# Optimization experiments

Hardware: AMD Instinct MI355X
Metric: run time of the kernel (lower is better)

## Reference

```python
import jax, jax.numpy as jnp
import numpy as np

EMBED_DIM = 768
NUM_HEADS = 12
MAX_LEN = 512
BATCH = 8
SEQ = 512
HEAD_DIM = EMBED_DIM // NUM_HEADS


def setup_inputs() -> dict:
    key = jax.random.key(0)
    ks = jax.random.split(key, 7)
    x = jax.random.normal(ks[0], (BATCH, SEQ, EMBED_DIM), dtype=jnp.float32)
    mask = jnp.ones((BATCH, SEQ), dtype=jnp.int32)
    Wq = jax.random.normal(ks[1], (EMBED_DIM, EMBED_DIM), dtype=jnp.float32) * (1.0 / np.sqrt(EMBED_DIM))
    Wk = jax.random.normal(ks[2], (EMBED_DIM, EMBED_DIM), dtype=jnp.float32) * (1.0 / np.sqrt(EMBED_DIM))
    Wv = jax.random.normal(ks[3], (EMBED_DIM, EMBED_DIM), dtype=jnp.float32) * (1.0 / np.sqrt(EMBED_DIM))
    rel_pos = jax.random.normal(ks[4], (2 * MAX_LEN - 1, NUM_HEADS), dtype=jnp.float32)
    Wo = jax.random.normal(ks[5], (EMBED_DIM, EMBED_DIM), dtype=jnp.float32) * (1.0 / np.sqrt(EMBED_DIM))
    bo = jax.random.normal(ks[6], (EMBED_DIM,), dtype=jnp.float32) * 0.02
    return {"x": x, "mask": mask, "Wq": Wq, "Wk": Wk, "Wv": Wv,
            "rel_pos": rel_pos, "Wo": Wo, "bo": bo}


def reference(x, mask, Wq, Wk, Wv, rel_pos, Wo, bo):
    B, S, E = x.shape
    H, D = NUM_HEADS, HEAD_DIM
    Q = (x @ Wq).reshape(B, S, H, D)
    K = (x @ Wk).reshape(B, S, H, D)
    V = (x @ Wv).reshape(B, S, H, D)
    # scores: [B, H, S, S]
    scores = jnp.einsum('bqhd,bkhd->bhqk', Q, K) / np.sqrt(D).astype(np.float32)
    # relative position bias: idx[q,k] = k - q + max_len - 1, clamped
    pos = jnp.arange(S)
    idx = jnp.clip(pos[None, :] - pos[:, None] + MAX_LEN - 1, 0, 2 * MAX_LEN - 2)
    bias = rel_pos[idx]                       # [S, S, H]
    scores = scores + jnp.transpose(bias, (2, 0, 1))[None]  # [1,H,S,S]
    # mask: b i * b j -> [B,1,S,S]
    m2 = (mask[:, None, :, None] * mask[:, None, None, :]) != 0
    mask_value = -jnp.finfo(scores.dtype).max
    scores = jnp.where(m2, scores, mask_value)
    attn = jax.nn.softmax(scores, axis=-1)
    out = jnp.einsum('bhqk,bkhd->bqhd', attn, V).reshape(B, S, E)
    out = out @ Wo + bo  # dropout is identity in eval mode
    return out
```

## Files before the change

kernel.cpp:

```cpp
#include <hip/hip_runtime.h>
#include <hip/hip_bf16.h>
#include <cfloat>
#include <cstdint>
#include <cmath>

#define EMBED 768
#define NHEAD 12
#define SEQB  8
#define SEQ   512
#define HDIM  64
#define WMAT  589824

typedef __attribute__((ext_vector_type(8))) short short8;
typedef __attribute__((ext_vector_type(4))) short short4v;
typedef __attribute__((ext_vector_type(4))) float f32x4;

__device__ __forceinline__ short f2bf(float f) {
  uint32_t u = __float_as_uint(f);
  u += 0x7FFF + ((u >> 16) & 1u);
  return (short)(u >> 16);
}

__device__ __forceinline__ short f2bf1(float f) {
  int r;
  asm("v_cvt_pk_bf16_f32 %0, %1, %2" : "=v"(r) : "v"(f), "v"(f));
  return (short)r;
}

__device__ __forceinline__ void gload_lds16(const void* g, void* l) {
  __builtin_amdgcn_global_load_lds((const __attribute__((address_space(1))) void*)g,
                                   (__attribute__((address_space(3))) void*)l, 16, 0, 0);
}

__global__ void k_cast_x(const float* __restrict__ x, short* __restrict__ xb) {
  int i = blockIdx.x * blockDim.x + threadIdx.x;
  const int n4 = SEQB * SEQ * EMBED / 4;
  if (i < n4) {
    float4 v = ((const float4*)x)[i];
    short4v o;
    o.x = f2bf(v.x); o.y = f2bf(v.y); o.z = f2bf(v.z); o.w = f2bf(v.w);
    ((short4v*)xb)[i] = o;
  }
}

__global__ void k_cast_wt(const float* __restrict__ Wq, const float* __restrict__ Wk,
                          const float* __restrict__ Wv, const float* __restrict__ Wo,
                          short* __restrict__ Wt) {
  __shared__ float tile[32][33];
  const int mat = blockIdx.z;
  const float* src = (mat == 0) ? Wq : (mat == 1) ? Wk : (mat == 2) ? Wv : Wo;
  const int n0 = blockIdx.x * 32, k0 = blockIdx.y * 32;
  const int tx = threadIdx.x & 31, ty = threadIdx.x >> 5;
  #pragma unroll
  for (int rr = 0; rr < 4; rr++)
    tile[ty + rr * 8][tx] = src[(size_t)(k0 + ty + rr * 8) * EMBED + n0 + tx];
  __syncthreads();
  short* dst = Wt + (size_t)mat * WMAT;
  #pragma unroll
  for (int rr = 0; rr < 4; rr++)
    dst[(size_t)(n0 + ty + rr * 8) * EMBED + k0 + tx] = f2bf(tile[tx][ty + rr * 8]);
}

template <int MODE>
__launch_bounds__(256)
__global__ void k_gemm(const short* __restrict__ A, const short* __restrict__ B,
                       short* __restrict__ O0, short* __restrict__ O1,
                       short* __restrict__ O2,
                       float* __restrict__ OF, const float* __restrict__ bias) {
  __shared__ __attribute__((aligned(16))) short As[128 * 32];
  __shared__ __attribute__((aligned(16))) short Bs[128 * 32];
  const int tid = threadIdx.x;
  const int lane = tid & 63, w = tid >> 6;
  const int g = lane >> 4, c = lane & 15;
  const int wi = (w >> 1) * 64, wj = (w & 1) * 64;
  const int i0 = blockIdx.y * 128, j0 = blockIdx.x * 128;

  f32x4 acc[4][4];
  #pragma unroll
  for (int a = 0; a < 4; a++)
    #pragma unroll
    for (int b2 = 0; b2 < 4; b2++) acc[a][b2] = (f32x4){0.f, 0.f, 0.f, 0.f};

  for (int k0 = 0; k0 < EMBED; k0 += 32) {
    if (k0) __syncthreads();
    #pragma unroll
    for (int it = 0; it < 2; it++) {
      int gi = tid + it * 256;
      int row = gi >> 2, q = gi & 3;
      gload_lds16(A + (size_t)(i0 + row) * EMBED + k0 + q * 8, As + gi * 8);
      gload_lds16(B + (size_t)(j0 + row) * EMBED + k0 + q * 8, Bs + gi * 8);
    }
    __syncthreads();
    short8 aF[4], bF[4];
    #pragma unroll
    for (int mi = 0; mi < 4; mi++) aF[mi] = *(const short8*)&As[(wi + mi * 16 + c) * 32 + g * 8];
    #pragma unroll
    for (int nj = 0; nj < 4; nj++) bF[nj] = *(const short8*)&Bs[(wj + nj * 16 + c) * 32 + g * 8];
    #pragma unroll
    for (int mi = 0; mi < 4; mi++)
      #pragma unroll
      for (int nj = 0; nj < 4; nj++)
        acc[mi][nj] = __builtin_amdgcn_mfma_f32_16x16x32_bf16(aF[mi], bF[nj], acc[mi][nj], 0, 0, 0);
  }

  #pragma unroll
  for (int mi = 0; mi < 4; mi++) {
    int i = i0 + wi + mi * 16 + 4 * g;
    #pragma unroll
    for (int nj = 0; nj < 4; nj++) {
      int j = j0 + wj + nj * 16 + c;
      f32x4 v = acc[mi][nj];
      if (MODE == 0) {
        int n = i, m = j;
        int b = m >> 9, s = m & 511;
        if (n < 1536) {
          short* dst = O0; int nn = n;
          if (n >= 768) { dst = O1; nn -= 768; }
          int h = nn >> 6, d = nn & 63;
          short4v o; o.x = f2bf(v.x); o.y = f2bf(v.y); o.z = f2bf(v.z); o.w = f2bf(v.w);
          *(short4v*)&dst[(size_t)(((b * 12 + h) * 512 + s) * 64 + d)] = o;
        } else {
          int nn = n - 1536;
          int h = nn >> 6, d = nn & 63;
          size_t base = ((size_t)(b * 12 + h) * 64 + d) * 512 + s;
          O2[base] = f2bf(v.x); O2[base + 512] = f2bf(v.y);
          O2[base + 1024] = f2bf(v.z); O2[base + 1536] = f2bf(v.w);
        }
      } else {
        int n = i, m = j;
        float4 bb = *(const float4*)&bias[n];
        float4 o; o.x = v.x + bb.x; o.y = v.y + bb.y; o.z = v.z + bb.z; o.w = v.w + bb.w;
        *(float4*)&OF[(size_t)m * EMBED + n] = o;
      }
    }
  }
}

__launch_bounds__(256)
__global__ void k_attn(const short* __restrict__ Q, const short* __restrict__ K,
                       const short* __restrict__ Vt, const int* __restrict__ mask,
                       const float* __restrict__ rel_pos, short* __restrict__ attO) {
  __shared__ float bias_lds[1024];
  __shared__ int mask_lds[512];
  __shared__ __attribute__((aligned(16))) short Plds[4][16 * 32];
  __shared__ __attribute__((aligned(16))) short Kbuf[2][32 * 64];
  __shared__ __attribute__((aligned(16))) short Vbuf[2][64 * 32];
  const int tid = threadIdx.x;
  const int lane = tid & 63, w = tid >> 6;
  const int g = lane >> 4, c = lane & 15;
  const int bid = blockIdx.x;
  const int q0 = (bid / 96) * 64;
  const int bh = bid % 96;
  const int b = bh / 12, h = bh % 12;
  const short* Qb = Q + (size_t)bh * (512 * 64);
  const short* Kb = K + (size_t)bh * (512 * 64);
  const short* Vb = Vt + (size_t)bh * (64 * 512);

  const float LOG2E = 1.44269504089f;
  for (int i = tid; i < 1023; i += 256) bias_lds[i] = (rel_pos[i * 12 + h] - 16.0f) * LOG2E;
  for (int i = tid; i < 512; i += 256) mask_lds[i] = mask[b * 512 + i];

  const int krow_s = tid >> 3, kc_s = tid & 7;
  const int vrow_s = tid >> 2, vc_s = tid & 3;
  #define STAGEKV(T, BUF)                                                             \
    {                                                                                 \
      gload_lds16(Kb + ((T) * 32 + krow_s) * 64 + (kc_s ^ (krow_s & 7)) * 8,          \
                  &Kbuf[BUF][tid * 8]);                                               \
      gload_lds16(Vb + (size_t)vrow_s * 512 + (T) * 32 + (vc_s ^ ((vrow_s >> 1) & 3)) * 8, \
                  &Vbuf[BUF][tid * 8]);                                               \
    }

  STAGEKV(0, 0)

  short8 qf[2];
  #pragma unroll
  for (int dc = 0; dc < 2; dc++)
    qf[dc] = *(const short8*)&Qb[(q0 + w * 16 + c) * 64 + dc * 32 + g * 8];

  __syncthreads();

  int qrow[4], mq[4], bbase[4];
  #pragma unroll
  for (int r = 0; r < 4; r++) {
    qrow[r] = q0 + w * 16 + 4 * g + r;
    mq[r] = mask_lds[qrow[r]];
    bbase[r] = 511 - qrow[r];
  }

  float l_part[4];
  f32x4 accO[4];
  #pragma unroll
  for (int r = 0; r < 4; r++) l_part[r] = 0.f;
  #pragma unroll
  for (int dt = 0; dt < 4; dt++) accO[dt] = (f32x4){0.f, 0.f, 0.f, 0.f};

  const float SC = 0.125f * 1.44269504089f;
  short* Pw = &Plds[w][0];
  const int rdoff = c * 32 + g * 8;
  const int kswz = c & 7;
  const int vswz = (c >> 1) & 3;

  int bufsel = 0;
  for (int t = 0; t < 16; ++t) {
    if (t < 15) STAGEKV(t + 1, bufsel ^ 1)
    const short* Kt = &Kbuf[bufsel][0];
    const short* Vs = &Vbuf[bufsel][0];

    short8 kf[4], vf[4];
    #pragma unroll
    for (int ct = 0; ct < 2; ct++)
      #pragma unroll
      for (int dc = 0; dc < 2; dc++)
        kf[ct * 2 + dc] = *(const short8*)&Kt[(ct * 16 + c) * 64 + ((dc * 4 + g) ^ kswz) * 8];
    #pragma unroll
    for (int dt = 0; dt < 4; dt++)
      vf[dt] = *(const short8*)&Vs[(dt * 16 + c) * 32 + ((g ^ vswz)) * 8];

    f32x4 s0 = (f32x4){0.f, 0.f, 0.f, 0.f}, s1 = s0;
    s0 = __builtin_amdgcn_mfma_f32_16x16x32_bf16(qf[0], kf[0], s0, 0, 0, 0);
    s0 = __builtin_amdgcn_mfma_f32_16x16x32_bf16(qf[1], kf[1], s0, 0, 0, 0);
    s1 = __builtin_amdgcn_mfma_f32_16x16x32_bf16(qf[0], kf[2], s1, 0, 0, 0);
    s1 = __builtin_amdgcn_mfma_f32_16x16x32_bf16(qf[1], kf[3], s1, 0, 0, 0);

    float p_[2][4];
    {
      const int krow = t * 32 + c;
      const int mk0 = mask_lds[krow], mk1 = mask_lds[krow + 16];
      #pragma unroll
      for (int r = 0; r < 4; r++) {
        float a0 = fmaf(s0[r], SC, bias_lds[krow + bbase[r]]);
        float a1 = fmaf(s1[r], SC, bias_lds[krow + 16 + bbase[r]]);
        float p0 = exp2f(a0), p1 = exp2f(a1);
        if ((mq[r] & mk0) == 0) p0 = 0.f;
        if ((mq[r] & mk1) == 0) p1 = 0.f;
        p_[0][r] = p0; p_[1][r] = p1;
        l_part[r] += p0 + p1;
      }
    }
    #pragma unroll
    for (int ct = 0; ct < 2; ct++)
      #pragma unroll
      for (int r = 0; r < 4; r++)
        Pw[(4 * g + r) * 32 + ct * 16 + c] = f2bf1(p_[ct][r]);
    short8 pa = *(const short8*)&Pw[rdoff];
    #pragma unroll
    for (int dt = 0; dt < 4; dt++)
      accO[dt] = __builtin_amdgcn_mfma_f32_16x16x32_bf16(pa, vf[dt], accO[dt], 0, 0, 0);

    __syncthreads();
    bufsel ^= 1;
  }

  float inv[4];
  #pragma unroll
  for (int r = 0; r < 4; r++) {
    float lr = l_part[r];
    #pragma unroll
    for (int off = 1; off < 16; off <<= 1) lr += __shfl_xor(lr, off);
    inv[r] = 1.0f / lr;
  }
  #pragma unroll
  for (int dt = 0; dt < 4; dt++)
    #pragma unroll
    for (int r = 0; r < 4; r++)
      attO[(size_t)(b * 512 + qrow[r]) * EMBED + h * 64 + dt * 16 + c] =
          f2bf(accO[dt][r] * inv[r]);
}

extern "C" void kernel_launch(void* const* d_in, const int* in_sizes, int n_in,
                              void* d_out, int out_size, void* d_ws, size_t ws_size,
                              hipStream_t stream) {
  const float* x = (const float*)d_in[0];
  const int* mask = (const int*)d_in[1];
  const float* Wq = (const float*)d_in[2];
  const float* Wk = (const float*)d_in[3];
  const float* Wv = (const float*)d_in[4];
  const float* rel_pos = (const float*)d_in[5];
  const float* Wo = (const float*)d_in[6];
  const float* bo = (const float*)d_in[7];
  float* out = (float*)d_out;

  char* ws = (char*)d_ws;
  short* xb = (short*)ws;
  short* Wt = (short*)(ws + 6291456);
  short* Qg = (short*)(ws + 6291456 + 4718592);
  short* Kg = Qg + 3145728;
  short* Vt = Kg + 3145728;
  short* attO = xb;

  k_cast_x<<<3072, 256, 0, stream>>>(x, xb);
  k_cast_wt<<<dim3(24, 24, 4), 256, 0, stream>>>(Wq, Wk, Wv, Wo, Wt);
  k_gemm<0><<<dim3(32, 18), 256, 0, stream>>>(Wt, xb, Qg, Kg, Vt, nullptr, nullptr);
  k_attn<<<768, 256, 0, stream>>>(Qg, Kg, Vt, mask, rel_pos, attO);
  k_gemm<2><<<dim3(32, 6), 256, 0, stream>>>(Wt + 3 * WMAT, attO, nullptr, nullptr, nullptr, out, bo);
}
```

Before: 153.8 us.

## Double-buffer GEMM LDS tiles and use partial vmcnt waits in attention

The projection GEMM now stages its A/B tiles into two LDS buffers, prefetching the next K-step while computing the current one. It uses s_waitcnt vmcnt(N) with raw s_barrier instead of full __syncthreads. The attention kernel's K/V double-buffering likewise switches to partial vmcnt waits, so the prefetch for tile t+1 can stay in flight while tile t is consumed. This targets exposed global-load latency, at the cost of doubled GEMM LDS use and correctness that depends on hand-counted outstanding-load numbers.

```diff
diff --git a/kernel.cpp b/kernel.cpp
--- a/kernel.cpp
+++ b/kernel.cpp
@@ -67,13 +67,14 @@
                        short* __restrict__ O0, short* __restrict__ O1,
                        short* __restrict__ O2,
                        float* __restrict__ OF, const float* __restrict__ bias) {
-  __shared__ __attribute__((aligned(16))) short As[128 * 32];
-  __shared__ __attribute__((aligned(16))) short Bs[128 * 32];
+  __shared__ __attribute__((aligned(16))) short As[2][128 * 32];
+  __shared__ __attribute__((aligned(16))) short Bs[2][128 * 32];
   const int tid = threadIdx.x;
   const int lane = tid & 63, w = tid >> 6;
   const int g = lane >> 4, c = lane & 15;
   const int wi = (w >> 1) * 64, wj = (w & 1) * 64;
   const int i0 = blockIdx.y * 128, j0 = blockIdx.x * 128;
+  const int NSTEP = EMBED / 32;
 
   f32x4 acc[4][4];
   #pragma unroll
@@ -81,26 +82,45 @@
     #pragma unroll
     for (int b2 = 0; b2 < 4; b2++) acc[a][b2] = (f32x4){0.f, 0.f, 0.f, 0.f};
 
-  for (int k0 = 0; k0 < EMBED; k0 += 32) {
-    if (k0) __syncthreads();
-    #pragma unroll
-    for (int it = 0; it < 2; it++) {
-      int gi = tid + it * 256;
-      int row = gi >> 2, q = gi & 3;
-      gload_lds16(A + (size_t)(i0 + row) * EMBED + k0 + q * 8, As + gi * 8);
-      gload_lds16(B + (size_t)(j0 + row) * EMBED + k0 + q * 8, Bs + gi * 8);
-    }
-    __syncthreads();
+  #define GSTAGE(S, BUF)                                                            \
+    { _Pragma("unroll")                                                             \
+      for (int it = 0; it < 2; it++) {                                              \
+        int gi = tid + it * 256;                                                    \
+        int row = gi >> 2, qq = gi & 3;                                             \
+        gload_lds16(A + (size_t)(i0 + row) * EMBED + (S) * 32 + qq * 8,             \
+                    &As[BUF][gi * 8]);                                              \
+        gload_lds16(B + (size_t)(j0 + row) * EMBED + (S) * 32 + qq * 8,             \
+                    &Bs[BUF][gi * 8]);                                              \
+      } }
+
+  GSTAGE(0, 0)
+  __syncthreads();
+
+  for (int s = 0; s < NSTEP; ++s) {
+    const int cur = s & 1;
+    if (s < NSTEP - 1) {
+      GSTAGE(s + 1, cur ^ 1)
+      asm volatile("s_waitcnt vmcnt(4)" ::: "memory");
+    } else {
+      asm volatile("s_waitcnt vmcnt(0)" ::: "memory");
+    }
+    __builtin_amdgcn_sched_barrier(0);
+    __builtin_amdgcn_s_barrier();
+    __builtin_amdgcn_sched_barrier(0);
+
     short8 aF[4], bF[4];
     #pragma unroll
-    for (int mi = 0; mi < 4; mi++) aF[mi] = *(const short8*)&As[(wi + mi * 16 + c) * 32 + g * 8];
-    #pragma unroll
-    for (int nj = 0; nj < 4; nj++) bF[nj] = *(const short8*)&Bs[(wj + nj * 16 + c) * 32 + g * 8];
+    for (int mi = 0; mi < 4; mi++) aF[mi] = *(const short8*)&As[cur][(wi + mi * 16 + c) * 32 + g * 8];
+    #pragma unroll
+    for (int nj = 0; nj < 4; nj++) bF[nj] = *(const short8*)&Bs[cur][(wj + nj * 16 + c) * 32 + g * 8];
     #pragma unroll
     for (int mi = 0; mi < 4; mi++)
       #pragma unroll
       for (int nj = 0; nj < 4; nj++)
         acc[mi][nj] = __builtin_amdgcn_mfma_f32_16x16x32_bf16(aF[mi], bF[nj], acc[mi][nj], 0, 0, 0);
+
+    __builtin_amdgcn_s_barrier();
+    __builtin_amdgcn_sched_barrier(0);
   }
 
   #pragma unroll
@@ -200,11 +220,20 @@
   const int kswz = c & 7;
   const int vswz = (c >> 1) & 3;
 
-  int bufsel = 0;
   for (int t = 0; t < 16; ++t) {
-    if (t < 15) STAGEKV(t + 1, bufsel ^ 1)
-    const short* Kt = &Kbuf[bufsel][0];
-    const short* Vs = &Vbuf[bufsel][0];
+    const int cur = t & 1;
+    if (t < 15) {
+      STAGEKV(t + 1, cur ^ 1)
+      asm volatile("s_waitcnt vmcnt(2)" ::: "memory");
+    } else {
+      asm volatile("s_waitcnt vmcnt(0)" ::: "memory");
+    }
+    __builtin_amdgcn_sched_barrier(0);
+    __builtin_amdgcn_s_barrier();
+    __builtin_amdgcn_sched_barrier(0);
+
+    const short* Kt = &Kbuf[cur][0];
+    const short* Vs = &Vbuf[cur][0];
 
     short8 kf[4], vf[4];
     #pragma unroll
@@ -247,8 +276,8 @@
     for (int dt = 0; dt < 4; dt++)
       accO[dt] = __builtin_amdgcn_mfma_f32_16x16x32_bf16(pa, vf[dt], accO[dt], 0, 0, 0);
 
-    __syncthreads();
-    bufsel ^= 1;
+    __builtin_amdgcn_s_barrier();
+    __builtin_amdgcn_sched_barrier(0);
   }
 
   float inv[4];
```

Result: no change. 155.6 us (+1.2%).
